# Optimization experiments

Measured on AMD Instinct MI355X. Metric: run time of the kernel, lower is better.

Reference implementation:

```python
import jax, jax.numpy as jnp
import numpy as np

GROUPS = 4

def shuffle(t):
    # torch Shuffle: transpose(-1,-2).contiguous().view(original_shape)
    return jnp.swapaxes(t, -1, -2).reshape(t.shape)

def setup_inputs() -> dict:
    key = jax.random.key(0)
    B, H = 131072, 512
    gh = 2 * H // GROUPS  # 256
    k = jax.random.split(key, 5)
    s = lambda fan_in: 1.0 / np.sqrt(fan_in)
    x = jax.random.normal(k[0], (B, H), dtype=jnp.float32)
    # weights stored as (in, out); Linear has bias=False throughout
    W1 = jax.random.uniform(k[1], (H, H), jnp.float32, -s(H), s(H))
    W2 = jax.random.uniform(k[2], (gh, gh), jnp.float32, -s(gh), s(gh))
    W3 = jax.random.uniform(k[3], (gh, gh), jnp.float32, -s(gh), s(gh))
    W4 = jax.random.uniform(k[4], (2 * H, H), jnp.float32, -s(2 * H), s(2 * H))
    return {"x": x, "W1": W1, "W2": W2, "W3": W3, "W4": W4}

def reference(x, W1, W2, W3, W4):
    B, H = x.shape
    gh = 2 * H // GROUPS
    sorted_x = jnp.sort(x, axis=1, stable=True)
    h = jnp.stack((x, sorted_x), axis=1)          # (B, 2, H)
    h = h @ W1                                    # (B, 2, H)
    h = h.reshape(B, GROUPS, gh)                  # Flatten + Unflatten
    h = shuffle(h)
    h = h @ W2                                    # (B, GROUPS, gh)
    h = shuffle(h)
    h = jax.nn.relu(h @ W3)                       # (B, GROUPS, gh)
    h = h.reshape(B, GROUPS * gh)                 # (B, 2H)
    scores = jax.nn.sigmoid(h @ W4)               # (B, H)
    return x * scores
```

## Files before the change

### kernel.cpp

```cpp
#include <hip/hip_runtime.h>
#include <hip/hip_bf16.h>
#include <cstdint>
#include <cstddef>

typedef short bf16x8 __attribute__((ext_vector_type(8)));
typedef float f32x4 __attribute__((ext_vector_type(4)));

#define BM 128
#define BN 128
#define BK 32
#define NBUF 3

__device__ __forceinline__ void gl_lds16(const __hip_bfloat16* gp, __hip_bfloat16* lp) {
  __builtin_amdgcn_global_load_lds((const __attribute__((address_space(1))) void*)gp,
                                   (__attribute__((address_space(3))) void*)lp, 16, 0, 0);
}

__global__ void __launch_bounds__(256) wtrans_kernel(const float* __restrict__ src,
                                                     __hip_bfloat16* __restrict__ dst,
                                                     int R, int C) {
  int idx = blockIdx.x * 256 + threadIdx.x;
  if (idx >= R * C) return;
  int r = idx / C, c = idx % C;
  dst[(size_t)c * R + r] = __float2bfloat16(src[idx]);
}

__global__ void __launch_bounds__(256) sort_kernel(const float* __restrict__ x,
                                                   __hip_bfloat16* __restrict__ h0) {
  int row = blockIdx.x * 4 + (threadIdx.x >> 6);
  int lane = threadIdx.x & 63;
  const float* xr = x + (size_t)row * 512;

  float v[8];
  *(float4*)&v[0] = *(const float4*)&xr[lane * 8];
  *(float4*)&v[4] = *(const float4*)&xr[lane * 8 + 4];

  __hip_bfloat16* h = h0 + (size_t)row * 1024;
  {
    alignas(16) __hip_bfloat16 ob[8];
#pragma unroll
    for (int i = 0; i < 8; ++i) ob[i] = __float2bfloat16(v[i]);
    *(bf16x8*)&h[lane * 8] = *(const bf16x8*)ob;
  }

#pragma unroll
  for (int k = 2; k <= 512; k <<= 1) {
#pragma unroll
    for (int j = k >> 1; j > 0; j >>= 1) {
      if (j >= 8) {
        int L = j >> 3;
        bool lower = (lane & L) == 0;
        bool up = (((lane * 8) & k) == 0);
        bool sel = (lower == up);
#pragma unroll
        for (int r = 0; r < 8; ++r) {
          float pv = __shfl_xor(v[r], L, 64);
          float mn = fminf(v[r], pv), mx = fmaxf(v[r], pv);
          v[r] = sel ? mn : mx;
        }
      } else {
#pragma unroll
        for (int r = 0; r < 8; ++r) {
          if ((r & j) == 0) {
            int r2 = r | j;
            bool up = ((((lane * 8) + r) & k) == 0);
            float a = v[r], b = v[r2];
            float mn = fminf(a, b), mx = fmaxf(a, b);
            v[r] = up ? mn : mx;
            v[r2] = up ? mx : mn;
          }
        }
      }
    }
  }

  {
    alignas(16) __hip_bfloat16 ob[8];
#pragma unroll
    for (int i = 0; i < 8; ++i) ob[i] = __float2bfloat16(v[i]);
    *(bf16x8*)&h[512 + lane * 8] = *(const bf16x8*)ob;
  }
}

template <int EPI>
__global__ void __launch_bounds__(256) gemm_k(const __hip_bfloat16* __restrict__ A,
                                              const __hip_bfloat16* __restrict__ BT,
                                              __hip_bfloat16* __restrict__ Cb,
                                              float* __restrict__ Co,
                                              const float* __restrict__ X,
                                              int M, int N, int K) {
  __shared__ __hip_bfloat16 lA[NBUF][BM * BK];
  __shared__ __hip_bfloat16 lB[NBUF][BN * BK];

  int nwg = gridDim.x;
  int bid = blockIdx.x;
  int cpx = nwg >> 3;
  int wg = (bid & 7) * cpx + (bid >> 3);

  int nt_tiles = N / BN;
  int m0 = (wg / nt_tiles) * BM;
  int n0 = (wg % nt_tiles) * BN;

  int tid = threadIdx.x;
  int lane = tid & 63;
  int w = tid >> 6;
  int wm = (w >> 1) << 6;
  int wn = (w & 1) << 6;
  int r16 = lane & 15;
  int k8 = (lane >> 4) << 3;

  int colA = (lane & 3) * 8;
  int rsub = lane >> 2;
  int row0 = w * 16 + rsub;
  int row1 = (4 + w) * 16 + rsub;

  f32x4 acc[4][4] = {};

#define STAGE(t, buf)                                                          \
  do {                                                                         \
    int k0_ = (t) * BK;                                                        \
    gl_lds16(&A[(size_t)(m0 + row0) * K + k0_ + colA], &lA[buf][w * 512]);     \
    gl_lds16(&A[(size_t)(m0 + row1) * K + k0_ + colA], &lA[buf][(4 + w) * 512]); \
    gl_lds16(&BT[(size_t)(n0 + row0) * K + k0_ + colA], &lB[buf][w * 512]);    \
    gl_lds16(&BT[(size_t)(n0 + row1) * K + k0_ + colA], &lB[buf][(4 + w) * 512]); \
  } while (0)

  int nt = K / BK;
  STAGE(0, 0);
  STAGE(1, 1);
  asm volatile("s_waitcnt vmcnt(4)" ::: "memory");
  __builtin_amdgcn_s_barrier();

  int cur = 0;
  for (int t = 0; t < nt; ++t) {
    int nb = cur + 2; if (nb >= NBUF) nb -= NBUF;
    if (t + 2 < nt) STAGE(t + 2, nb);

    bf16x8 af[4], bfr[4];
#pragma unroll
    for (int i = 0; i < 4; ++i)
      af[i] = *(const bf16x8*)&lA[cur][(wm + 16 * i + r16) * BK + k8];
#pragma unroll
    for (int j = 0; j < 4; ++j)
      bfr[j] = *(const bf16x8*)&lB[cur][(wn + 16 * j + r16) * BK + k8];
#pragma unroll
    for (int i = 0; i < 4; ++i)
#pragma unroll
      for (int j = 0; j < 4; ++j)
        acc[i][j] = __builtin_amdgcn_mfma_f32_16x16x32_bf16(af[i], bfr[j], acc[i][j], 0, 0, 0);

    if (t + 2 < nt) {
      asm volatile("s_waitcnt vmcnt(4)" ::: "memory");
    } else if (t + 1 < nt) {
      asm volatile("s_waitcnt vmcnt(0)" ::: "memory");
    }
    if (t + 1 < nt) __builtin_amdgcn_s_barrier();
    cur = (cur + 1 == NBUF) ? 0 : cur + 1;
  }
#undef STAGE

#pragma unroll
  for (int i = 0; i < 4; ++i) {
    int grow_base = m0 + wm + 16 * i + ((lane >> 4) << 2);
#pragma unroll
    for (int j = 0; j < 4; ++j) {
      int gcol = n0 + wn + 16 * j + (lane & 15);
#pragma unroll
      for (int r = 0; r < 4; ++r) {
        int grow = grow_base + r;
        float v = acc[i][j][r];
        if constexpr (EPI == 1) {
          int b = grow >> 1, p = grow & 1;
          Cb[(size_t)b * 1024 + 4 * (gcol & 255) + (p << 1) + (gcol >> 8)] = __float2bfloat16(v);
        } else if constexpr (EPI == 2) {
          int b = grow >> 2, g = grow & 3;
          Cb[(size_t)b * 1024 + 4 * gcol + g] = __float2bfloat16(v);
        } else if constexpr (EPI == 3) {
          Cb[(size_t)grow * N + gcol] = __float2bfloat16(fmaxf(v, 0.f));
        } else {
          float xv = X[(size_t)grow * N + gcol];
          Co[(size_t)grow * N + gcol] = xv / (1.f + __expf(-v));
        }
      }
    }
  }
}

extern "C" void kernel_launch(void* const* d_in, const int* in_sizes, int n_in,
                              void* d_out, int out_size, void* d_ws, size_t ws_size,
                              hipStream_t stream) {
  const float* x  = (const float*)d_in[0];
  const float* W1 = (const float*)d_in[1];
  const float* W2 = (const float*)d_in[2];
  const float* W3 = (const float*)d_in[3];
  const float* W4 = (const float*)d_in[4];

  const int B = 131072;

  char* ws = (char*)d_ws;
  __hip_bfloat16* W1T = (__hip_bfloat16*)(ws);
  __hip_bfloat16* W2T = (__hip_bfloat16*)(ws + 524288);
  __hip_bfloat16* W3T = (__hip_bfloat16*)(ws + 655360);
  __hip_bfloat16* W4T = (__hip_bfloat16*)(ws + 786432);
  __hip_bfloat16* bufA = (__hip_bfloat16*)(ws + 2097152);
  __hip_bfloat16* bufB = bufA + (size_t)134217728;

  wtrans_kernel<<<(512 * 512) / 256, 256, 0, stream>>>(W1, W1T, 512, 512);
  wtrans_kernel<<<(256 * 256) / 256, 256, 0, stream>>>(W2, W2T, 256, 256);
  wtrans_kernel<<<(256 * 256) / 256, 256, 0, stream>>>(W3, W3T, 256, 256);
  wtrans_kernel<<<(1024 * 512) / 256, 256, 0, stream>>>(W4, W4T, 1024, 512);

  sort_kernel<<<B / 4, 256, 0, stream>>>(x, bufA);

  gemm_k<1><<<(2 * B / BM) * (512 / BN), 256, 0, stream>>>(bufA, W1T, bufB, nullptr, nullptr,
                                                           2 * B, 512, 512);
  gemm_k<2><<<(4 * B / BM) * (256 / BN), 256, 0, stream>>>(bufB, W2T, bufA, nullptr, nullptr,
                                                           4 * B, 256, 256);
  gemm_k<3><<<(4 * B / BM) * (256 / BN), 256, 0, stream>>>(bufA, W3T, bufB, nullptr, nullptr,
                                                           4 * B, 256, 256);
  gemm_k<4><<<(B / BM) * (512 / BN), 256, 0, stream>>>(bufB, W4T, nullptr, (float*)d_out, x,
                                                       B, 512, 1024);
}
```

Baseline: 1.119 ms.

## Deepen GEMM pipeline to four LDS buffers with compile-time shapes and full unroll

The GEMM main loop moves from a 3-buffer to a 4-buffer LDS ring with three stages in flight, and the next stage is now issued after the LDS fragment reads. N and K become template parameters so the k-loop can be fully unrolled, buffer indices become constants, and per-row global pointers are hoisted out of the loop. The goal is to hide more global-load latency and remove index arithmetic. In exchange, LDS use rises from 48KB to 64KB per block, which may cut occupancy, and full unrolling grows code size.

```diff
diff --git a/kernel.cpp b/kernel.cpp
--- a/kernel.cpp
+++ b/kernel.cpp
@@ -9,7 +9,7 @@
 #define BM 128
 #define BN 128
 #define BK 32
-#define NBUF 3
+#define NBUF 4
 
 __device__ __forceinline__ void gl_lds16(const __hip_bfloat16* gp, __hip_bfloat16* lp) {
   __builtin_amdgcn_global_load_lds((const __attribute__((address_space(1))) void*)gp,
@@ -82,13 +82,12 @@
   }
 }
 
-template <int EPI>
+template <int EPI, int N, int K>
 __global__ void __launch_bounds__(256) gemm_k(const __hip_bfloat16* __restrict__ A,
                                               const __hip_bfloat16* __restrict__ BT,
                                               __hip_bfloat16* __restrict__ Cb,
                                               float* __restrict__ Co,
-                                              const float* __restrict__ X,
-                                              int M, int N, int K) {
+                                              const float* __restrict__ X) {
   __shared__ __hip_bfloat16 lA[NBUF][BM * BK];
   __shared__ __hip_bfloat16 lB[NBUF][BN * BK];
 
@@ -97,9 +96,9 @@
   int cpx = nwg >> 3;
   int wg = (bid & 7) * cpx + (bid >> 3);
 
-  int nt_tiles = N / BN;
-  int m0 = (wg / nt_tiles) * BM;
-  int n0 = (wg % nt_tiles) * BN;
+  constexpr int NT = N / BN;
+  int m0 = (wg / NT) * BM;
+  int n0 = (wg % NT) * BN;
 
   int tid = threadIdx.x;
   int lane = tid & 63;
@@ -114,28 +113,33 @@
   int row0 = w * 16 + rsub;
   int row1 = (4 + w) * 16 + rsub;
 
+  const __hip_bfloat16* gA0 = &A[(size_t)(m0 + row0) * K + colA];
+  const __hip_bfloat16* gA1 = &A[(size_t)(m0 + row1) * K + colA];
+  const __hip_bfloat16* gB0 = &BT[(size_t)(n0 + row0) * K + colA];
+  const __hip_bfloat16* gB1 = &BT[(size_t)(n0 + row1) * K + colA];
+
   f32x4 acc[4][4] = {};
 
-#define STAGE(t, buf)                                                          \
-  do {                                                                         \
-    int k0_ = (t) * BK;                                                        \
-    gl_lds16(&A[(size_t)(m0 + row0) * K + k0_ + colA], &lA[buf][w * 512]);     \
-    gl_lds16(&A[(size_t)(m0 + row1) * K + k0_ + colA], &lA[buf][(4 + w) * 512]); \
-    gl_lds16(&BT[(size_t)(n0 + row0) * K + k0_ + colA], &lB[buf][w * 512]);    \
-    gl_lds16(&BT[(size_t)(n0 + row1) * K + k0_ + colA], &lB[buf][(4 + w) * 512]); \
+#define STAGE(t)                                         \
+  do {                                                   \
+    int k0_ = (t) * BK;                                  \
+    int b_ = (t) & 3;                                    \
+    gl_lds16(gA0 + k0_, &lA[b_][w * 512]);               \
+    gl_lds16(gA1 + k0_, &lA[b_][(4 + w) * 512]);         \
+    gl_lds16(gB0 + k0_, &lB[b_][w * 512]);               \
+    gl_lds16(gB1 + k0_, &lB[b_][(4 + w) * 512]);         \
   } while (0)
 
-  int nt = K / BK;
-  STAGE(0, 0);
-  STAGE(1, 1);
-  asm volatile("s_waitcnt vmcnt(4)" ::: "memory");
+  constexpr int nt = K / BK;
+  STAGE(0);
+  STAGE(1);
+  STAGE(2);
+  asm volatile("s_waitcnt vmcnt(8)" ::: "memory");
   __builtin_amdgcn_s_barrier();
 
-  int cur = 0;
+#pragma unroll
   for (int t = 0; t < nt; ++t) {
-    int nb = cur + 2; if (nb >= NBUF) nb -= NBUF;
-    if (t + 2 < nt) STAGE(t + 2, nb);
-
+    const int cur = t & 3;
     bf16x8 af[4], bfr[4];
 #pragma unroll
     for (int i = 0; i < 4; ++i)
@@ -143,19 +147,22 @@
 #pragma unroll
     for (int j = 0; j < 4; ++j)
       bfr[j] = *(const bf16x8*)&lB[cur][(wn + 16 * j + r16) * BK + k8];
+
+    if (t + 3 < nt) STAGE(t + 3);
+
 #pragma unroll
     for (int i = 0; i < 4; ++i)
 #pragma unroll
       for (int j = 0; j < 4; ++j)
         acc[i][j] = __builtin_amdgcn_mfma_f32_16x16x32_bf16(af[i], bfr[j], acc[i][j], 0, 0, 0);
 
-    if (t + 2 < nt) {
-      asm volatile("s_waitcnt vmcnt(4)" ::: "memory");
-    } else if (t + 1 < nt) {
-      asm volatile("s_waitcnt vmcnt(0)" ::: "memory");
+    if (t + 1 < nt) {
+      const int rem = nt - 2 - t;
+      if (rem >= 2)      asm volatile("s_waitcnt vmcnt(8)" ::: "memory");
+      else if (rem == 1) asm volatile("s_waitcnt vmcnt(4)" ::: "memory");
+      else               asm volatile("s_waitcnt vmcnt(0)" ::: "memory");
+      __builtin_amdgcn_s_barrier();
     }
-    if (t + 1 < nt) __builtin_amdgcn_s_barrier();
-    cur = (cur + 1 == NBUF) ? 0 : cur + 1;
   }
 #undef STAGE
 
@@ -212,12 +219,8 @@
 
   sort_kernel<<<B / 4, 256, 0, stream>>>(x, bufA);
 
-  gemm_k<1><<<(2 * B / BM) * (512 / BN), 256, 0, stream>>>(bufA, W1T, bufB, nullptr, nullptr,
-                                                           2 * B, 512, 512);
-  gemm_k<2><<<(4 * B / BM) * (256 / BN), 256, 0, stream>>>(bufB, W2T, bufA, nullptr, nullptr,
-                                                           4 * B, 256, 256);
-  gemm_k<3><<<(4 * B / BM) * (256 / BN), 256, 0, stream>>>(bufA, W3T, bufB, nullptr, nullptr,
-                                                           4 * B, 256, 256);
-  gemm_k<4><<<(B / BM) * (512 / BN), 256, 0, stream>>>(bufB, W4T, nullptr, (float*)d_out, x,
-                                                       B, 512, 1024);
-}
+  gemm_k<1, 512, 512><<<(2 * B / BM) * (512 / BN), 256, 0, stream>>>(bufA, W1T, bufB, nullptr, nullptr);
+  gemm_k<2, 256, 256><<<(4 * B / BM) * (256 / BN), 256, 0, stream>>>(bufB, W2T, bufA, nullptr, nullptr);
+  gemm_k<3, 256, 256><<<(4 * B / BM) * (256 / BN), 256, 0, stream>>>(bufA, W3T, bufB, nullptr, nullptr);
+  gemm_k<4, 512, 1024><<<(B / BM) * (512 / BN), 256, 0, stream>>>(bufB, W4T, nullptr, (float*)d_out, x);
+}
```

Measured after the change: 1.285 ms. 14.9% more time.
